# Optimization experiments

Hardware: AMD Instinct MI355X
Metric: run time of the kernel (lower is better)

## Reference

```python
import jax, jax.numpy as jnp
import numpy as np

B, N_HEADS, D_MODEL, S = 4, 16, 128, 2048
SQRT_D = np.sqrt(D_MODEL).astype(np.float32)


def setup_inputs() -> dict:
    key = jax.random.key(0)
    kx, kq, kk, kv, kw = jax.random.split(key, 5)
    N = B * N_HEADS
    return {
        "x": jax.random.normal(kx, (B, D_MODEL, S), dtype=jnp.float32),
        "Q": jax.random.normal(kq, (N, D_MODEL, S), dtype=jnp.float32),
        "K": jax.random.normal(kk, (N, D_MODEL, S), dtype=jnp.float32),
        "V": jax.random.normal(kv, (N, D_MODEL, S), dtype=jnp.float32),
        "W": jax.random.normal(kw, (N_HEADS * D_MODEL, D_MODEL), dtype=jnp.float32) * 0.02,
    }


def reference(x, Q, K, V, W):
    # x contributes only its shape (the repeated copy is overwritten in the original)
    b, d_model, s = x.shape
    # scores[n, i, j] = sum_d Q[n, d, i] * K[n, d, j] / sqrt(d_model)
    scores = jnp.einsum("ndi,ndj->nij", Q, K) / SQRT_D  # [N, S, S]
    # legacy F.softmax (no dim) on a 3D tensor -> softmax over dim=1 (query index)
    attn = jax.nn.softmax(scores, axis=1)
    # out[n, d, j] = sum_i V[n, d, i] * attn[n, i, j]
    out = jnp.einsum("ndi,nij->ndj", V, attn)  # [N, d_model, S]
    out = out.reshape(b, N_HEADS * d_model, s)  # [B, H*d_model, S]
    # final projection: W^T @ out, W: [H*d_model, d_model]
    return jnp.einsum("hd,bhs->bds", W, out)  # [B, d_model, S]
```

## Files before the change

### kernel.cpp

```cpp
#include <hip/hip_runtime.h>
#include <hip/hip_bf16.h>

typedef unsigned short u16;
typedef unsigned int   u32;
typedef short  short8v __attribute__((ext_vector_type(8)));
typedef u16    u16x8   __attribute__((ext_vector_type(8)));
typedef float  f32x16  __attribute__((ext_vector_type(16)));
typedef float  f32x4v  __attribute__((ext_vector_type(4)));
typedef u32    u32x2   __attribute__((ext_vector_type(2)));
typedef u32    u32x4   __attribute__((ext_vector_type(4)));

#define HEADS 64
#define DMODEL 128
#define SEQ 2048

#define SCQ 0.1275293f
#define PSTR 80


__device__ __forceinline__ f32x16 mfma_bf16(short8v a, short8v b, f32x16 c) {
  return __builtin_amdgcn_mfma_f32_32x32x16_bf16(a, b, c, 0, 0, 0);
}

__device__ __forceinline__ f32x16 fzero16() {
  f32x16 z;
#pragma unroll
  for (int i = 0; i < 16; ++i) z[i] = 0.f;
  return z;
}

__device__ __forceinline__ float fast_exp2(float x) {
  float r;
  asm("v_exp_f32 %0, %1" : "=v"(r) : "v"(x));
  return r;
}

__device__ __forceinline__ u32 bfround(float x) {
  u32 u = __builtin_bit_cast(u32, x);
  u += 0x7fffu + ((u >> 16) & 1u);
  return u >> 16;
}
__device__ __forceinline__ u32 bfpair(float lo, float hi) {
  u32 a = __builtin_bit_cast(u32, lo); a += 0x7fffu + ((a >> 16) & 1u);
  u32 b = __builtin_bit_cast(u32, hi); b += 0x7fffu + ((b >> 16) & 1u);
  return (a >> 16) | (b & 0xffff0000u);
}
__device__ __forceinline__ u32 packbf(float lo, float hi) {
  u32 l16 = (u32)__builtin_bit_cast(u16, __float2bfloat16(lo));
  u32 h16 = (u32)__builtin_bit_cast(u16, __float2bfloat16(hi));
  return l16 | (h16 << 16);
}

typedef const __attribute__((address_space(1))) void* gp1_t;
typedef __attribute__((address_space(3))) void* lp3_t;
__device__ __forceinline__ void gload16(const u16* g, u16* l) {
  __builtin_amdgcn_global_load_lds((gp1_t)g, (lp3_t)l, 16, 0, 0);
}

__device__ __forceinline__ void stage_T(const float* __restrict__ src, int pos0,
                                        u16* lds, int tid) {
  int ic = tid & 7;
  int d0 = (tid >> 3) * 2;
  const float* p = src + d0 * SEQ + pos0 + ic * 8;
  f32x4v xa = *reinterpret_cast<const f32x4v*>(p);
  f32x4v xb = *reinterpret_cast<const f32x4v*>(p + 4);
  f32x4v ya = *reinterpret_cast<const f32x4v*>(p + SEQ);
  f32x4v yb = *reinterpret_cast<const f32x4v*>(p + SEQ + 4);
  u32* lds32 = reinterpret_cast<u32*>(lds);
  int cc = d0 >> 3;
#pragma unroll
  for (int k = 0; k < 8; ++k) {
    int r = ic * 8 + k;
    int c2 = cc ^ (r & 15);
    float xv = (k < 4) ? xa[k & 3] : xb[k & 3];
    float yv = (k < 4) ? ya[k & 3] : yb[k & 3];
    lds32[(r * 128 + c2 * 8 + (d0 & 7)) >> 1] = bfpair(xv, yv);
  }
}

__device__ __forceinline__ short8v ld_at(const u16* lds, int row, int chunk) {
  return *reinterpret_cast<const short8v*>(lds + row * 128 + ((chunk ^ (row & 15)) * 8));
}
__device__ __forceinline__ short8v ld_vt(const u16* lds, int d, int chunk) {
  return *reinterpret_cast<const short8v*>(lds + d * 64 + ((chunk ^ (d & 7)) * 8));
}

__global__ __launch_bounds__(256) void prep_kernel(
    const float* __restrict__ Q, const float* __restrict__ V,
    const float* __restrict__ Wsrc, u16* __restrict__ Qt,
    u16* __restrict__ V16t, u16* __restrict__ Wt) {
  int blk = blockIdx.x;
  int t = threadIdx.x;
  if (blk < 2048) {
    int n = blk >> 5, pt = blk & 31;
    const float* src = Q + (size_t)n * DMODEL * SEQ;
    u16* dst = Qt + (size_t)n * SEQ * DMODEL + (size_t)pt * 64 * DMODEL;
    int pq = t & 15, dq = t >> 4;
#pragma unroll
    for (int p = 0; p < 2; ++p) {
      int d0 = (dq + 16 * p) * 4;
      const float* s0 = src + (size_t)d0 * SEQ + pt * 64 + pq * 4;
      f32x4v r0 = *reinterpret_cast<const f32x4v*>(s0);
      f32x4v r1 = *reinterpret_cast<const f32x4v*>(s0 + SEQ);
      f32x4v r2 = *reinterpret_cast<const f32x4v*>(s0 + 2 * SEQ);
      f32x4v r3 = *reinterpret_cast<const f32x4v*>(s0 + 3 * SEQ);
#pragma unroll
      for (int j = 0; j < 4; ++j) {
        u32x2 v = { bfpair(r0[j] * SCQ, r1[j] * SCQ), bfpair(r2[j] * SCQ, r3[j] * SCQ) };
        *reinterpret_cast<u32x2*>(dst + (pq * 4 + j) * DMODEL + d0) = v;
      }
    }
  } else if (blk < 4096) {
    int b2 = blk - 2048;
    int n = b2 >> 5, it = b2 & 31;
    int s8 = (t & 7) * 8;
    const float* src = V + (size_t)n * DMODEL * SEQ + it * 64 + s8;
    u16* dst = V16t + (size_t)b2 * DMODEL * 64 + s8;
#pragma unroll
    for (int rr = 0; rr < 4; ++rr) {
      int d = (t >> 3) + 32 * rr;
      const float* p = src + (size_t)d * SEQ;
      f32x4v a = *reinterpret_cast<const f32x4v*>(p);
      f32x4v b = *reinterpret_cast<const f32x4v*>(p + 4);
      u32x4 v = { bfpair(a[0], a[1]), bfpair(a[2], a[3]),
                  bfpair(b[0], b[1]), bfpair(b[2], b[3]) };
      *reinterpret_cast<u32x4*>(dst + d * 64) = v;
    }
  } else {
    int e = (blk - 4096) * 256 + t;
#pragma unroll
    for (int rr = 0; rr < 2; ++rr) {
      int o = e + rr * 131072;
      int dm = o >> 11, c = o & 2047;
      Wt[o] = (u16)bfround(Wsrc[c * 128 + dm]);
    }
  }
}

__global__ __launch_bounds__(1024, 4) void attn_kernel(
    const u16* __restrict__ Qt, const float* __restrict__ K,
    const u16* __restrict__ V16t, u16* __restrict__ Ows) {
  __shared__ __align__(16) u16 AT2[2][64 * DMODEL];
  __shared__ __align__(16) u16 VT2[2][DMODEL * 64];
  __shared__ __align__(16) u16 PB[2][256 * PSTR];
  __shared__ float AL[2][256];
  __shared__ float LL[256];
  const int tid = threadIdx.x;
  const int w = tid >> 6;
  const int lane = tid & 63;
  const int g = lane >> 5;
  const int lj = lane & 31;
  const int p_ = blockIdx.x;
  const int n = ((p_ >> 6) << 3) | (p_ & 7);
  const int j0 = ((p_ >> 3) & 7) * 256;
  const u16* Qtn = Qt + (size_t)n * SEQ * DMODEL;
  const float* Kb = K + (size_t)n * DMODEL * SEQ;
  const u16* Vtn = V16t + (size_t)n * 32 * DMODEL * 64;

  int qoff[2], voff[2];
#pragma unroll
  for (int i = 0; i < 2; ++i) {
    int idx = (w & 7) * 2 + i;
    int pos = idx * 4 + (lane >> 4);
    qoff[i] = pos * DMODEL + (((lane & 15) ^ (pos & 15)) * 8);
    int d = idx * 8 + (lane >> 3);
    voff[i] = d * 64 + (((lane & 7) ^ (d & 7)) * 8);
  }

  if (w < 8) {
    const u16* qb = Qtn;
#pragma unroll
    for (int i = 0; i < 2; ++i)
      gload16(qb + qoff[i], AT2[0] + ((w & 7) * 2 + i) * 512);
  }
  short8v bq[8];
  u16* KS = PB[0];
#pragma unroll 1
  for (int p = 0; p < 4; ++p) {
    if (tid < 512) stage_T(Kb, j0 + p * 64, KS, tid);
    __syncthreads();
    if (w < 8 && (w >> 1) == p) {
      int row = (w & 1) * 32 + lj;
#pragma unroll
      for (int c = 0; c < 8; ++c) bq[c] = ld_at(KS, row, 2 * c + g);
    }
    __syncthreads();
  }

  if (w < 8) {
    float m_run = -1e30f, l_run = 0.f;
    const int prow = w * 32 + lj;
    u16* const prowbase0 = PB[0] + prow * PSTR;
    u16* const prowbase1 = PB[1] + prow * PSTR;
    const int swz = prow & 7;

#pragma unroll 1
    for (int t = 0; t <= 32; ++t) {
      if (t < 32) {
        const u16* qb = Qtn + (size_t)((t + 1) & 31) * (64 * DMODEL);
        u16* ab = AT2[(t + 1) & 1];
#pragma unroll
        for (int i = 0; i < 2; ++i)
          gload16(qb + qoff[i], ab + ((w & 7) * 2 + i) * 512);

        const u16* curAT = AT2[t & 1];
        f32x16 c0 = fzero16(), c1 = fzero16();
        __builtin_amdgcn_s_setprio(1);
#pragma unroll
        for (int dc = 0; dc < 8; ++dc) {
          short8v a0 = ld_at(curAT, lj, 2 * dc + g);
          short8v a1 = ld_at(curAT, 32 + lj, 2 * dc + g);
          c0 = mfma_bf16(a0, bq[dc], c0);
          c1 = mfma_bf16(a1, bq[dc], c1);
        }
        __builtin_amdgcn_s_setprio(0);

        float m8[8];
#pragma unroll
        for (int r = 0; r < 8; ++r)
          m8[r] = fmaxf(fmaxf(c0[r], c0[r + 8]), fmaxf(c1[r], c1[r + 8]));
#pragma unroll
        for (int r = 0; r < 4; ++r) m8[r] = fmaxf(m8[r], m8[r + 4]);
        float mx = fmaxf(fmaxf(m8[0], m8[1]), fmaxf(m8[2], m8[3]));
        mx = fmaxf(mx, __shfl_xor(mx, 32, 64));

        float al = 1.0f;
        if (!__all(mx <= m_run + 8.f)) {
          float mn = fmaxf(m_run, mx);
          al = fast_exp2(m_run - mn);
          m_run = mn;
          l_run *= al;
        }
        if (!g) AL[t & 1][prow] = al;

#pragma unroll
        for (int r = 0; r < 16; ++r) c0[r] = fast_exp2(c0[r] - m_run);
#pragma unroll
        for (int r = 0; r < 16; ++r) c1[r] = fast_exp2(c1[r] - m_run);
        float s8[8];
#pragma unroll
        for (int r = 0; r < 8; ++r) s8[r] = (c0[r] + c0[r + 8]) + (c1[r] + c1[r + 8]);
#pragma unroll
        for (int r = 0; r < 4; ++r) s8[r] += s8[r + 4];
        float ps = (s8[0] + s8[1]) + (s8[2] + s8[3]);
        ps += __shfl_xor(ps, 32, 64);
        l_run += ps;

        u16* pdst = (t & 1) ? prowbase1 : prowbase0;
#pragma unroll
        for (int half = 0; half < 2; ++half) {
#pragma unroll
          for (int q = 0; q < 4; ++q) {
            u32x2 val;
            val.x = half ? packbf(c1[4 * q + 0], c1[4 * q + 1])
                         : packbf(c0[4 * q + 0], c0[4 * q + 1]);
            val.y = half ? packbf(c1[4 * q + 2], c1[4 * q + 3])
                         : packbf(c0[4 * q + 2], c0[4 * q + 3]);
            int G = q + 4 * half;
            *reinterpret_cast<u32x2*>(pdst + ((G ^ swz) << 3) + 4 * g) = val;
          }
        }
      }
      __syncthreads();
    }
    if (!g) LL[prow] = l_run;
    __syncthreads();
  } else {
    f32x16 o0 = fzero16(), o1 = fzero16(), o2 = fzero16(), o3 = fzero16();
    const int prow = (w - 8) * 32 + lj;
    const int swz = prow & 7;

#pragma unroll 1
    for (int t = 0; t <= 32; ++t) {
      if (t < 32) {
        const u16* vb = Vtn + (size_t)t * (DMODEL * 64);
        u16* vbuf = VT2[t & 1];
#pragma unroll
        for (int i = 0; i < 2; ++i)
          gload16(vb + voff[i], vbuf + ((w & 7) * 2 + i) * 512);
      }
      if (t >= 1) {
        const int tp = t - 1;
        const u16* curVT = VT2[tp & 1];
        const u16* prowp = PB[tp & 1] + prow * PSTR;
        float al = AL[tp & 1][prow];
        if (!__all(al == 1.0f)) {
#pragma unroll
          for (int r = 0; r < 16; ++r) { o0[r] *= al; o1[r] *= al; o2[r] *= al; o3[r] *= al; }
        }
        __builtin_amdgcn_s_setprio(1);
#pragma unroll
        for (int kc = 0; kc < 4; ++kc) {
          short8v pf = *reinterpret_cast<const short8v*>(
              prowp + (((2 * kc + g) ^ swz) << 3));
          short8v v0 = ld_vt(curVT, lj,      2 * kc + g);
          short8v v1 = ld_vt(curVT, 32 + lj, 2 * kc + g);
          short8v v2 = ld_vt(curVT, 64 + lj, 2 * kc + g);
          short8v v3 = ld_vt(curVT, 96 + lj, 2 * kc + g);
          o0 = mfma_bf16(v0, pf, o0);
          o1 = mfma_bf16(v1, pf, o1);
          o2 = mfma_bf16(v2, pf, o2);
          o3 = mfma_bf16(v3, pf, o3);
        }
        __builtin_amdgcn_s_setprio(0);
      }
      __syncthreads();
    }
    __syncthreads();
    float inv = 1.f / LL[prow];
    int jme = j0 + prow;
    u16* obase = Ows + ((size_t)n * SEQ + jme) * DMODEL;
#define STORE_OT(OV, DT)                                                  \
    {                                                                     \
      _Pragma("unroll") for (int q = 0; q < 4; ++q) {                     \
        int d0 = (DT) * 32 + 4 * g + 8 * q;                               \
        u32x2 val;                                                        \
        val.x = bfpair(OV[4 * q + 0] * inv, OV[4 * q + 1] * inv);         \
        val.y = bfpair(OV[4 * q + 2] * inv, OV[4 * q + 3] * inv);         \
        *reinterpret_cast<u32x2*>(obase + d0) = val;                      \
      }                                                                   \
    }
    STORE_OT(o0, 0) STORE_OT(o1, 1) STORE_OT(o2, 2) STORE_OT(o3, 3)
#undef STORE_OT
  }
}

__global__ __launch_bounds__(256) void proj_kernel(
    const u16* __restrict__ Ows, const u16* __restrict__ Wt, float* __restrict__ out) {
  __shared__ __align__(16) u16 BT[32 * 128];
  const int tid = threadIdx.x;
  const int w = tid >> 6, lane = tid & 63, g = lane >> 5, lj = lane & 31;
  const int b = blockIdx.x >> 6;
  const int j0 = (blockIdx.x & 63) * 32;
  f32x16 acc = fzero16();
#pragma unroll 1
  for (int h = 0; h < 16; ++h) {
    __syncthreads();
#pragma unroll
    for (int rr = 0; rr < 2; ++rr) {
      int s = tid + rr * 256;
      int r = s >> 4, cc = s & 15;
      u16x8 v = *reinterpret_cast<const u16x8*>(
          Ows + ((size_t)(b * 16 + h) * SEQ + j0 + r) * DMODEL + cc * 8);
      *reinterpret_cast<u16x8*>(BT + r * 128 + ((cc ^ (r & 7)) * 8)) = v;
    }
    __syncthreads();
#pragma unroll
    for (int kc = 0; kc < 8; ++kc) {
      short8v a = *reinterpret_cast<const short8v*>(
          Wt + (size_t)(w * 32 + lj) * SEQ + h * 128 + kc * 16 + g * 8);
      short8v bb = *reinterpret_cast<const short8v*>(
          BT + lj * 128 + (((2 * kc + g) ^ (lj & 7)) * 8));
      acc = mfma_bf16(a, bb, acc);
    }
  }
#pragma unroll
  for (int q = 0; q < 4; ++q) {
#pragma unroll
    for (int r = 0; r < 4; ++r) {
      int dm = w * 32 + 4 * g + 8 * q + r;
      out[((size_t)b * DMODEL + dm) * SEQ + j0 + lj] = acc[4 * q + r];
    }
  }
}

extern "C" void kernel_launch(void* const* d_in, const int* in_sizes, int n_in,
                              void* d_out, int out_size, void* d_ws, size_t ws_size,
                              hipStream_t stream) {
  (void)in_sizes; (void)n_in; (void)out_size; (void)ws_size;
  const float* Q = (const float*)d_in[1];
  const float* K = (const float*)d_in[2];
  const float* V = (const float*)d_in[3];
  const float* W = (const float*)d_in[4];
  const size_t NEL = (size_t)HEADS * SEQ * DMODEL;
  u16* Qt   = (u16*)d_ws;
  u16* V16t = Qt + NEL;
  u16* Ows  = V16t + NEL;
  u16* Wt   = Ows + NEL;
  float* out = (float*)d_out;

  prep_kernel<<<dim3(4608), dim3(256), 0, stream>>>(Q, V, W, Qt, V16t, Wt);
  attn_kernel<<<dim3(512), dim3(1024), 0, stream>>>(Qt, K, V16t, Ows);
  proj_kernel<<<dim3(256), dim3(256), 0, stream>>>(Ows, Wt, out);
}
```

Measured before the change: 234.7 us.

## Rebalance attention block to 4 softmax waves and 8 PV waves with 2x2 tiling

The attention block shrinks from 16 waves (8 score/softmax, 8 PV) to 12 waves: 4 producer waves each handle two 32-key column groups and process query rows in two 32-row halves, and 8 consumer waves each compute a 64x64 output tile (two key groups by two d-halves) instead of a 32x128 strip. The alpha rescale buffer gains a sub-step dimension so the consumers can apply per-half rescales. The aim is to reuse A and V fragments across two MFMAs, cut LDS reads per MFMA, and move more score work onto fewer waves with more registers each. The risk is that the 4 softmax waves become the critical path, and that occupancy drops to 3 blocks.

```diff
diff --git a/kernel.cpp b/kernel.cpp
--- a/kernel.cpp
+++ b/kernel.cpp
@@ -137,13 +137,13 @@
   }
 }
 
-__global__ __launch_bounds__(1024, 4) void attn_kernel(
+__global__ __launch_bounds__(768, 3) void attn_kernel(
     const u16* __restrict__ Qt, const float* __restrict__ K,
     const u16* __restrict__ V16t, u16* __restrict__ Ows) {
   __shared__ __align__(16) u16 AT2[2][64 * DMODEL];
   __shared__ __align__(16) u16 VT2[2][DMODEL * 64];
   __shared__ __align__(16) u16 PB[2][256 * PSTR];
-  __shared__ float AL[2][256];
+  __shared__ float AL[2][2][256];
   __shared__ float LL[256];
   const int tid = threadIdx.x;
   const int w = tid >> 6;
@@ -157,42 +157,52 @@
   const float* Kb = K + (size_t)n * DMODEL * SEQ;
   const u16* Vtn = V16t + (size_t)n * 32 * DMODEL * 64;
 
-  int qoff[2], voff[2];
-#pragma unroll
-  for (int i = 0; i < 2; ++i) {
-    int idx = (w & 7) * 2 + i;
+  int qoff[4];
+#pragma unroll
+  for (int i = 0; i < 4; ++i) {
+    int idx = (w & 3) * 4 + i;
     int pos = idx * 4 + (lane >> 4);
     qoff[i] = pos * DMODEL + (((lane & 15) ^ (pos & 15)) * 8);
+  }
+  int voff[2];
+#pragma unroll
+  for (int i = 0; i < 2; ++i) {
+    int idx = ((w - 4) & 7) * 2 + i;
     int d = idx * 8 + (lane >> 3);
     voff[i] = d * 64 + (((lane & 7) ^ (d & 7)) * 8);
   }
 
-  if (w < 8) {
-    const u16* qb = Qtn;
-#pragma unroll
-    for (int i = 0; i < 2; ++i)
-      gload16(qb + qoff[i], AT2[0] + ((w & 7) * 2 + i) * 512);
-  }
-  short8v bq[8];
+  if (w < 4) {
+#pragma unroll
+    for (int i = 0; i < 4; ++i)
+      gload16(Qtn + qoff[i], AT2[0] + ((w & 3) * 4 + i) * 512);
+  }
+
+  short8v bq0[8], bq1[8];
   u16* KS = PB[0];
 #pragma unroll 1
   for (int p = 0; p < 4; ++p) {
     if (tid < 512) stage_T(Kb, j0 + p * 64, KS, tid);
     __syncthreads();
-    if (w < 8 && (w >> 1) == p) {
+    if (w < 4) {
       int row = (w & 1) * 32 + lj;
-#pragma unroll
-      for (int c = 0; c < 8; ++c) bq[c] = ld_at(KS, row, 2 * c + g);
-    }
-    __syncthreads();
-  }
-
-  if (w < 8) {
-    float m_run = -1e30f, l_run = 0.f;
-    const int prow = w * 32 + lj;
-    u16* const prowbase0 = PB[0] + prow * PSTR;
-    u16* const prowbase1 = PB[1] + prow * PSTR;
-    const int swz = prow & 7;
+      if ((w >> 1) == p) {
+#pragma unroll
+        for (int c = 0; c < 8; ++c) bq0[c] = ld_at(KS, row, 2 * c + g);
+      }
+      if ((w >> 1) + 2 == p) {
+#pragma unroll
+        for (int c = 0; c < 8; ++c) bq1[c] = ld_at(KS, row, 2 * c + g);
+      }
+    }
+    __syncthreads();
+  }
+
+  if (w < 4) {
+    float m0 = -1e30f, l0 = 0.f, m1 = -1e30f, l1 = 0.f;
+    const int ja = w * 32 + lj;
+    const int jb = 128 + w * 32 + lj;
+    const int swza = ja & 7, swzb = jb & 7;
 
 #pragma unroll 1
     for (int t = 0; t <= 32; ++t) {
@@ -200,75 +210,74 @@
         const u16* qb = Qtn + (size_t)((t + 1) & 31) * (64 * DMODEL);
         u16* ab = AT2[(t + 1) & 1];
 #pragma unroll
-        for (int i = 0; i < 2; ++i)
-          gload16(qb + qoff[i], ab + ((w & 7) * 2 + i) * 512);
+        for (int i = 0; i < 4; ++i)
+          gload16(qb + qoff[i], ab + ((w & 3) * 4 + i) * 512);
 
         const u16* curAT = AT2[t & 1];
-        f32x16 c0 = fzero16(), c1 = fzero16();
-        __builtin_amdgcn_s_setprio(1);
-#pragma unroll
-        for (int dc = 0; dc < 8; ++dc) {
-          short8v a0 = ld_at(curAT, lj, 2 * dc + g);
-          short8v a1 = ld_at(curAT, 32 + lj, 2 * dc + g);
-          c0 = mfma_bf16(a0, bq[dc], c0);
-          c1 = mfma_bf16(a1, bq[dc], c1);
+        u16* pda = PB[t & 1] + ja * PSTR;
+        u16* pdb = PB[t & 1] + jb * PSTR;
+
+#pragma unroll
+        for (int s = 0; s < 2; ++s) {
+          f32x16 c0 = fzero16(), c1 = fzero16();
+          __builtin_amdgcn_s_setprio(1);
+#pragma unroll
+          for (int dc = 0; dc < 8; ++dc) {
+            short8v a = ld_at(curAT, s * 32 + lj, 2 * dc + g);
+            c0 = mfma_bf16(a, bq0[dc], c0);
+            c1 = mfma_bf16(a, bq1[dc], c1);
+          }
+          __builtin_amdgcn_s_setprio(0);
+
+#define SOFTPACK(C, M, L, JROW, SWZ, PD)                                     \
+          {                                                                  \
+            float t8[8];                                                     \
+            _Pragma("unroll") for (int r = 0; r < 8; ++r)                    \
+                t8[r] = fmaxf(C[r], C[r + 8]);                               \
+            _Pragma("unroll") for (int r = 0; r < 4; ++r)                    \
+                t8[r] = fmaxf(t8[r], t8[r + 4]);                             \
+            float mx = fmaxf(fmaxf(t8[0], t8[1]), fmaxf(t8[2], t8[3]));      \
+            mx = fmaxf(mx, __shfl_xor(mx, 32, 64));                          \
+            float al = 1.0f;                                                 \
+            if (!__all(mx <= (M) + 8.f)) {                                   \
+              float mn = fmaxf((M), mx);                                     \
+              al = fast_exp2((M)-mn);                                        \
+              (M) = mn; (L) *= al;                                           \
+            }                                                                \
+            if (!g) AL[t & 1][s][JROW] = al;                                 \
+            _Pragma("unroll") for (int r = 0; r < 16; ++r)                   \
+                C[r] = fast_exp2(C[r] - (M));                                \
+            _Pragma("unroll") for (int r = 0; r < 8; ++r)                    \
+                t8[r] = C[r] + C[r + 8];                                     \
+            _Pragma("unroll") for (int r = 0; r < 4; ++r)                    \
+                t8[r] += t8[r + 4];                                          \
+            float ps = (t8[0] + t8[1]) + (t8[2] + t8[3]);                    \
+            ps += __shfl_xor(ps, 32, 64);                                    \
+            (L) += ps;                                                       \
+            _Pragma("unroll") for (int q = 0; q < 4; ++q) {                  \
+              u32x2 val = { packbf(C[4 * q + 0], C[4 * q + 1]),              \
+                            packbf(C[4 * q + 2], C[4 * q + 3]) };            \
+              *reinterpret_cast<u32x2*>(                                     \
+                  (PD) + (((4 * s + q) ^ (SWZ)) << 3) + 4 * g) = val;        \
+            }                                                                \
+          }
+          SOFTPACK(c0, m0, l0, ja, swza, pda)
+          SOFTPACK(c1, m1, l1, jb, swzb, pdb)
+#undef SOFTPACK
         }
-        __builtin_amdgcn_s_setprio(0);
-
-        float m8[8];
-#pragma unroll
-        for (int r = 0; r < 8; ++r)
-          m8[r] = fmaxf(fmaxf(c0[r], c0[r + 8]), fmaxf(c1[r], c1[r + 8]));
-#pragma unroll
-        for (int r = 0; r < 4; ++r) m8[r] = fmaxf(m8[r], m8[r + 4]);
-        float mx = fmaxf(fmaxf(m8[0], m8[1]), fmaxf(m8[2], m8[3]));
-        mx = fmaxf(mx, __shfl_xor(mx, 32, 64));
-
-        float al = 1.0f;
-        if (!__all(mx <= m_run + 8.f)) {
-          float mn = fmaxf(m_run, mx);
-          al = fast_exp2(m_run - mn);
-          m_run = mn;
-          l_run *= al;
-        }
-        if (!g) AL[t & 1][prow] = al;
-
-#pragma unroll
-        for (int r = 0; r < 16; ++r) c0[r] = fast_exp2(c0[r] - m_run);
-#pragma unroll
-        for (int r = 0; r < 16; ++r) c1[r] = fast_exp2(c1[r] - m_run);
-        float s8[8];
-#pragma unroll
-        for (int r = 0; r < 8; ++r) s8[r] = (c0[r] + c0[r + 8]) + (c1[r] + c1[r + 8]);
-#pragma unroll
-        for (int r = 0; r < 4; ++r) s8[r] += s8[r + 4];
-        float ps = (s8[0] + s8[1]) + (s8[2] + s8[3]);
-        ps += __shfl_xor(ps, 32, 64);
-        l_run += ps;
-
-        u16* pdst = (t & 1) ? prowbase1 : prowbase0;
-#pragma unroll
-        for (int half = 0; half < 2; ++half) {
-#pragma unroll
-          for (int q = 0; q < 4; ++q) {
-            u32x2 val;
-            val.x = half ? packbf(c1[4 * q + 0], c1[4 * q + 1])
-                         : packbf(c0[4 * q + 0], c0[4 * q + 1]);
-            val.y = half ? packbf(c1[4 * q + 2], c1[4 * q + 3])
-                         : packbf(c0[4 * q + 2], c0[4 * q + 3]);
-            int G = q + 4 * half;
-            *reinterpret_cast<u32x2*>(pdst + ((G ^ swz) << 3) + 4 * g) = val;
-          }
-        }
       }
       __syncthreads();
     }
-    if (!g) LL[prow] = l_run;
+    if (!g) { LL[ja] = l0; LL[jb] = l1; }
     __syncthreads();
   } else {
-    f32x16 o0 = fzero16(), o1 = fzero16(), o2 = fzero16(), o3 = fzero16();
-    const int prow = (w - 8) * 32 + lj;
-    const int swz = prow & 7;
+    f32x16 oa0 = fzero16(), oa1 = fzero16(), ob0 = fzero16(), ob1 = fzero16();
+    const int cw = w - 4;
+    const int u = cw & 3, dh = cw >> 2;
+    const int ja = 64 * u + lj;
+    const int jb = ja + 32;
+    const int swza = ja & 7, swzb = jb & 7;
+    const int dbase = dh * 64;
 
 #pragma unroll 1
     for (int t = 0; t <= 32; ++t) {
@@ -277,50 +286,58 @@
         u16* vbuf = VT2[t & 1];
 #pragma unroll
         for (int i = 0; i < 2; ++i)
-          gload16(vb + voff[i], vbuf + ((w & 7) * 2 + i) * 512);
+          gload16(vb + voff[i], vbuf + (cw * 2 + i) * 512);
       }
       if (t >= 1) {
         const int tp = t - 1;
         const u16* curVT = VT2[tp & 1];
-        const u16* prowp = PB[tp & 1] + prow * PSTR;
-        float al = AL[tp & 1][prow];
-        if (!__all(al == 1.0f)) {
-#pragma unroll
-          for (int r = 0; r < 16; ++r) { o0[r] *= al; o1[r] *= al; o2[r] *= al; o3[r] *= al; }
+        const u16* pa = PB[tp & 1] + ja * PSTR;
+        const u16* pb = PB[tp & 1] + jb * PSTR;
+#pragma unroll
+        for (int s = 0; s < 2; ++s) {
+          float ala = AL[tp & 1][s][ja];
+          float alb = AL[tp & 1][s][jb];
+          if (!__all((ala == 1.0f) && (alb == 1.0f))) {
+#pragma unroll
+            for (int r = 0; r < 16; ++r) {
+              oa0[r] *= ala; oa1[r] *= ala; ob0[r] *= alb; ob1[r] *= alb;
+            }
+          }
+          __builtin_amdgcn_s_setprio(1);
+#pragma unroll
+          for (int kl = 0; kl < 2; ++kl) {
+            int G = 4 * s + 2 * kl + g;
+            short8v pfa = *reinterpret_cast<const short8v*>(pa + ((G ^ swza) << 3));
+            short8v pfb = *reinterpret_cast<const short8v*>(pb + ((G ^ swzb) << 3));
+            short8v v0 = ld_vt(curVT, dbase + lj, G);
+            short8v v1 = ld_vt(curVT, dbase + 32 + lj, G);
+            oa0 = mfma_bf16(v0, pfa, oa0);
+            oa1 = mfma_bf16(v1, pfa, oa1);
+            ob0 = mfma_bf16(v0, pfb, ob0);
+            ob1 = mfma_bf16(v1, pfb, ob1);
+          }
+          __builtin_amdgcn_s_setprio(0);
         }
-        __builtin_amdgcn_s_setprio(1);
-#pragma unroll
-        for (int kc = 0; kc < 4; ++kc) {
-          short8v pf = *reinterpret_cast<const short8v*>(
-              prowp + (((2 * kc + g) ^ swz) << 3));
-          short8v v0 = ld_vt(curVT, lj,      2 * kc + g);
-          short8v v1 = ld_vt(curVT, 32 + lj, 2 * kc + g);
-          short8v v2 = ld_vt(curVT, 64 + lj, 2 * kc + g);
-          short8v v3 = ld_vt(curVT, 96 + lj, 2 * kc + g);
-          o0 = mfma_bf16(v0, pf, o0);
-          o1 = mfma_bf16(v1, pf, o1);
-          o2 = mfma_bf16(v2, pf, o2);
-          o3 = mfma_bf16(v3, pf, o3);
-        }
-        __builtin_amdgcn_s_setprio(0);
       }
       __syncthreads();
     }
     __syncthreads();
-    float inv = 1.f / LL[prow];
-    int jme = j0 + prow;
-    u16* obase = Ows + ((size_t)n * SEQ + jme) * DMODEL;
-#define STORE_OT(OV, DT)                                                  \
+    float inva = 1.f / LL[ja];
+    float invb = 1.f / LL[jb];
+    u16* obase_a = Ows + ((size_t)n * SEQ + j0 + ja) * DMODEL;
+    u16* obase_b = Ows + ((size_t)n * SEQ + j0 + jb) * DMODEL;
+#define STORE_OT(OV, OB, DB, INV)                                         \
     {                                                                     \
       _Pragma("unroll") for (int q = 0; q < 4; ++q) {                     \
-        int d0 = (DT) * 32 + 4 * g + 8 * q;                               \
+        int d0 = dbase + (DB) * 32 + 4 * g + 8 * q;                       \
         u32x2 val;                                                        \
-        val.x = bfpair(OV[4 * q + 0] * inv, OV[4 * q + 1] * inv);         \
-        val.y = bfpair(OV[4 * q + 2] * inv, OV[4 * q + 3] * inv);         \
-        *reinterpret_cast<u32x2*>(obase + d0) = val;                      \
+        val.x = bfpair(OV[4 * q + 0] * (INV), OV[4 * q + 1] * (INV));     \
+        val.y = bfpair(OV[4 * q + 2] * (INV), OV[4 * q + 3] * (INV));     \
+        *reinterpret_cast<u32x2*>((OB) + d0) = val;                       \
       }                                                                   \
     }
-    STORE_OT(o0, 0) STORE_OT(o1, 1) STORE_OT(o2, 2) STORE_OT(o3, 3)
+    STORE_OT(oa0, obase_a, 0, inva) STORE_OT(oa1, obase_a, 1, inva)
+    STORE_OT(ob0, obase_b, 0, invb) STORE_OT(ob1, obase_b, 1, invb)
 #undef STORE_OT
   }
 }
@@ -380,6 +397,6 @@
   float* out = (float*)d_out;
 
   prep_kernel<<<dim3(4608), dim3(256), 0, stream>>>(Q, V, W, Qt, V16t, Wt);
-  attn_kernel<<<dim3(512), dim3(1024), 0, stream>>>(Qt, K, V16t, Ows);
+  attn_kernel<<<dim3(512), dim3(768), 0, stream>>>(Qt, K, V16t, Ows);
   proj_kernel<<<dim3(256), dim3(256), 0, stream>>>(Ows, Wt, out);
 }
```

Result: slower. 266.4 us (+13.5%).

## Halve attention block tiles to 512 threads with 32-row Q and V steps

Applied to the files above, without the earlier changes.

Each attention block now handles 128 key columns instead of 256, runs 512 threads (4 softmax waves, 4 PV waves), and steps through the query dimension in 32-row tiles over 64 iterations. The V prep layout becomes 32-wide tiles with a new swizzle, and the PV waves each cover two column groups and half of d_model so V fragments are reused. The grid doubles to 1024 blocks to improve occupancy and load balance and to shrink LDS per block, at the cost of twice as many loop iterations and barriers per block.

```diff
diff --git a/kernel.cpp b/kernel.cpp
--- a/kernel.cpp
+++ b/kernel.cpp
@@ -15,7 +15,7 @@
 #define SEQ 2048
 
 #define SCQ 0.1275293f
-#define PSTR 80
+#define PSTR 40
 
 
 __device__ __forceinline__ f32x16 mfma_bf16(short8v a, short8v b, f32x16 c) {
@@ -81,8 +81,9 @@
 __device__ __forceinline__ short8v ld_at(const u16* lds, int row, int chunk) {
   return *reinterpret_cast<const short8v*>(lds + row * 128 + ((chunk ^ (row & 15)) * 8));
 }
-__device__ __forceinline__ short8v ld_vt(const u16* lds, int d, int chunk) {
-  return *reinterpret_cast<const short8v*>(lds + d * 64 + ((chunk ^ (d & 7)) * 8));
+__device__ __forceinline__ short8v ld_vt32(const u16* lds, int d, int G) {
+  return *reinterpret_cast<const short8v*>(
+      lds + d * 32 + ((G ^ ((d ^ (d >> 2)) & 3)) * 8));
 }
 
 __global__ __launch_bounds__(256) void prep_kernel(
@@ -112,19 +113,19 @@
     }
   } else if (blk < 4096) {
     int b2 = blk - 2048;
-    int n = b2 >> 5, it = b2 & 31;
-    int s8 = (t & 7) * 8;
-    const float* src = V + (size_t)n * DMODEL * SEQ + it * 64 + s8;
-    u16* dst = V16t + (size_t)b2 * DMODEL * 64 + s8;
-#pragma unroll
-    for (int rr = 0; rr < 4; ++rr) {
-      int d = (t >> 3) + 32 * rr;
-      const float* p = src + (size_t)d * SEQ;
-      f32x4v a = *reinterpret_cast<const f32x4v*>(p);
-      f32x4v b = *reinterpret_cast<const f32x4v*>(p + 4);
+    int n = b2 >> 5, tp = b2 & 31;
+    int tile = tp * 2 + (t >> 7);
+    int d = t & 127;
+    const float* src = V + ((size_t)n * DMODEL + d) * SEQ + tile * 32;
+    u16* dst = V16t + (((size_t)n * 64 + tile) * DMODEL + d) * 32;
+    u32x4* dst16 = reinterpret_cast<u32x4*>(dst);
+#pragma unroll
+    for (int c = 0; c < 4; ++c) {
+      f32x4v a = *reinterpret_cast<const f32x4v*>(src + c * 8);
+      f32x4v b = *reinterpret_cast<const f32x4v*>(src + c * 8 + 4);
       u32x4 v = { bfpair(a[0], a[1]), bfpair(a[2], a[3]),
                   bfpair(b[0], b[1]), bfpair(b[2], b[3]) };
-      *reinterpret_cast<u32x4*>(dst + d * 64) = v;
+      dst16[c] = v;
     }
   } else {
     int e = (blk - 4096) * 256 + t;
@@ -137,49 +138,49 @@
   }
 }
 
-__global__ __launch_bounds__(1024, 4) void attn_kernel(
+__global__ __launch_bounds__(512, 4) void attn_kernel(
     const u16* __restrict__ Qt, const float* __restrict__ K,
     const u16* __restrict__ V16t, u16* __restrict__ Ows) {
-  __shared__ __align__(16) u16 AT2[2][64 * DMODEL];
-  __shared__ __align__(16) u16 VT2[2][DMODEL * 64];
-  __shared__ __align__(16) u16 PB[2][256 * PSTR];
-  __shared__ float AL[2][256];
-  __shared__ float LL[256];
+  __shared__ __align__(16) u16 AT2[2][32 * DMODEL];
+  __shared__ __align__(16) u16 VT2[2][DMODEL * 32];
+  __shared__ __align__(16) u16 PB[2][128 * PSTR];
+  __shared__ float AL[2][128];
+  __shared__ float LL[128];
   const int tid = threadIdx.x;
   const int w = tid >> 6;
   const int lane = tid & 63;
   const int g = lane >> 5;
   const int lj = lane & 31;
   const int p_ = blockIdx.x;
-  const int n = ((p_ >> 6) << 3) | (p_ & 7);
-  const int j0 = ((p_ >> 3) & 7) * 256;
+  const int n = ((p_ >> 7) << 3) | (p_ & 7);
+  const int j0 = ((p_ >> 3) & 15) * 128;
   const u16* Qtn = Qt + (size_t)n * SEQ * DMODEL;
   const float* Kb = K + (size_t)n * DMODEL * SEQ;
-  const u16* Vtn = V16t + (size_t)n * 32 * DMODEL * 64;
+  const u16* Vtn = V16t + (size_t)n * 64 * DMODEL * 32;
 
   int qoff[2], voff[2];
 #pragma unroll
   for (int i = 0; i < 2; ++i) {
-    int idx = (w & 7) * 2 + i;
+    int idx = (w & 3) * 2 + i;
     int pos = idx * 4 + (lane >> 4);
     qoff[i] = pos * DMODEL + (((lane & 15) ^ (pos & 15)) * 8);
-    int d = idx * 8 + (lane >> 3);
-    voff[i] = d * 64 + (((lane & 7) ^ (d & 7)) * 8);
-  }
-
-  if (w < 8) {
-    const u16* qb = Qtn;
+    int d = idx * 16 + (lane >> 2);
+    voff[i] = d * 32 + (((lane & 3) ^ ((d ^ (d >> 2)) & 3)) * 8);
+  }
+
+  if (w < 4) {
 #pragma unroll
     for (int i = 0; i < 2; ++i)
-      gload16(qb + qoff[i], AT2[0] + ((w & 7) * 2 + i) * 512);
-  }
+      gload16(Qtn + qoff[i], AT2[0] + ((w & 3) * 2 + i) * 512);
+  }
+
   short8v bq[8];
   u16* KS = PB[0];
 #pragma unroll 1
-  for (int p = 0; p < 4; ++p) {
-    if (tid < 512) stage_T(Kb, j0 + p * 64, KS, tid);
-    __syncthreads();
-    if (w < 8 && (w >> 1) == p) {
+  for (int p = 0; p < 2; ++p) {
+    stage_T(Kb, j0 + p * 64, KS, tid);
+    __syncthreads();
+    if (w < 4 && (w >> 1) == p) {
       int row = (w & 1) * 32 + lj;
 #pragma unroll
       for (int c = 0; c < 8; ++c) bq[c] = ld_at(KS, row, 2 * c + g);
@@ -187,41 +188,36 @@
     __syncthreads();
   }
 
-  if (w < 8) {
+  if (w < 4) {
     float m_run = -1e30f, l_run = 0.f;
-    const int prow = w * 32 + lj;
-    u16* const prowbase0 = PB[0] + prow * PSTR;
-    u16* const prowbase1 = PB[1] + prow * PSTR;
-    const int swz = prow & 7;
+    const int jrow = w * 32 + lj;
+    const int rotj = (jrow ^ (jrow >> 2)) & 3;
 
 #pragma unroll 1
-    for (int t = 0; t <= 32; ++t) {
-      if (t < 32) {
-        const u16* qb = Qtn + (size_t)((t + 1) & 31) * (64 * DMODEL);
+    for (int t = 0; t <= 64; ++t) {
+      if (t < 64) {
+        const u16* qb = Qtn + (size_t)((t + 1) & 63) * (32 * DMODEL);
         u16* ab = AT2[(t + 1) & 1];
 #pragma unroll
         for (int i = 0; i < 2; ++i)
-          gload16(qb + qoff[i], ab + ((w & 7) * 2 + i) * 512);
+          gload16(qb + qoff[i], ab + ((w & 3) * 2 + i) * 512);
 
         const u16* curAT = AT2[t & 1];
-        f32x16 c0 = fzero16(), c1 = fzero16();
+        f32x16 c0 = fzero16();
         __builtin_amdgcn_s_setprio(1);
 #pragma unroll
         for (int dc = 0; dc < 8; ++dc) {
-          short8v a0 = ld_at(curAT, lj, 2 * dc + g);
-          short8v a1 = ld_at(curAT, 32 + lj, 2 * dc + g);
-          c0 = mfma_bf16(a0, bq[dc], c0);
-          c1 = mfma_bf16(a1, bq[dc], c1);
+          short8v a = ld_at(curAT, lj, 2 * dc + g);
+          c0 = mfma_bf16(a, bq[dc], c0);
         }
         __builtin_amdgcn_s_setprio(0);
 
-        float m8[8];
-#pragma unroll
-        for (int r = 0; r < 8; ++r)
-          m8[r] = fmaxf(fmaxf(c0[r], c0[r + 8]), fmaxf(c1[r], c1[r + 8]));
-#pragma unroll
-        for (int r = 0; r < 4; ++r) m8[r] = fmaxf(m8[r], m8[r + 4]);
-        float mx = fmaxf(fmaxf(m8[0], m8[1]), fmaxf(m8[2], m8[3]));
+        float t8[8];
+#pragma unroll
+        for (int r = 0; r < 8; ++r) t8[r] = fmaxf(c0[r], c0[r + 8]);
+#pragma unroll
+        for (int r = 0; r < 4; ++r) t8[r] = fmaxf(t8[r], t8[r + 4]);
+        float mx = fmaxf(fmaxf(t8[0], t8[1]), fmaxf(t8[2], t8[3]));
         mx = fmaxf(mx, __shfl_xor(mx, 32, 64));
 
         float al = 1.0f;
@@ -231,96 +227,96 @@
           m_run = mn;
           l_run *= al;
         }
-        if (!g) AL[t & 1][prow] = al;
+        if (!g) AL[t & 1][jrow] = al;
 
 #pragma unroll
         for (int r = 0; r < 16; ++r) c0[r] = fast_exp2(c0[r] - m_run);
 #pragma unroll
-        for (int r = 0; r < 16; ++r) c1[r] = fast_exp2(c1[r] - m_run);
-        float s8[8];
-#pragma unroll
-        for (int r = 0; r < 8; ++r) s8[r] = (c0[r] + c0[r + 8]) + (c1[r] + c1[r + 8]);
-#pragma unroll
-        for (int r = 0; r < 4; ++r) s8[r] += s8[r + 4];
-        float ps = (s8[0] + s8[1]) + (s8[2] + s8[3]);
+        for (int r = 0; r < 8; ++r) t8[r] = c0[r] + c0[r + 8];
+#pragma unroll
+        for (int r = 0; r < 4; ++r) t8[r] += t8[r + 4];
+        float ps = (t8[0] + t8[1]) + (t8[2] + t8[3]);
         ps += __shfl_xor(ps, 32, 64);
         l_run += ps;
 
-        u16* pdst = (t & 1) ? prowbase1 : prowbase0;
-#pragma unroll
-        for (int half = 0; half < 2; ++half) {
-#pragma unroll
-          for (int q = 0; q < 4; ++q) {
-            u32x2 val;
-            val.x = half ? packbf(c1[4 * q + 0], c1[4 * q + 1])
-                         : packbf(c0[4 * q + 0], c0[4 * q + 1]);
-            val.y = half ? packbf(c1[4 * q + 2], c1[4 * q + 3])
-                         : packbf(c0[4 * q + 2], c0[4 * q + 3]);
-            int G = q + 4 * half;
-            *reinterpret_cast<u32x2*>(pdst + ((G ^ swz) << 3) + 4 * g) = val;
-          }
+        u16* pdst = PB[t & 1] + jrow * PSTR;
+#pragma unroll
+        for (int q = 0; q < 4; ++q) {
+          u32x2 val = { packbf(c0[4 * q + 0], c0[4 * q + 1]),
+                        packbf(c0[4 * q + 2], c0[4 * q + 3]) };
+          *reinterpret_cast<u32x2*>(pdst + ((q ^ rotj) << 3) + 4 * g) = val;
         }
       }
       __syncthreads();
     }
-    if (!g) LL[prow] = l_run;
+    if (!g) LL[jrow] = l_run;
     __syncthreads();
   } else {
-    f32x16 o0 = fzero16(), o1 = fzero16(), o2 = fzero16(), o3 = fzero16();
-    const int prow = (w - 8) * 32 + lj;
-    const int swz = prow & 7;
+    f32x16 oa0 = fzero16(), oa1 = fzero16(), ob0 = fzero16(), ob1 = fzero16();
+    const int cw = w - 4;
+    const int u = cw & 1, dh = cw >> 1;
+    const int ja = 64 * u + lj;
+    const int jb = ja + 32;
+    const int rota = (ja ^ (ja >> 2)) & 3;
+    const int rotb = (jb ^ (jb >> 2)) & 3;
+    const int dbase = dh * 64;
 
 #pragma unroll 1
-    for (int t = 0; t <= 32; ++t) {
-      if (t < 32) {
-        const u16* vb = Vtn + (size_t)t * (DMODEL * 64);
+    for (int t = 0; t <= 64; ++t) {
+      if (t < 64) {
+        const u16* vb = Vtn + (size_t)t * (DMODEL * 32);
         u16* vbuf = VT2[t & 1];
 #pragma unroll
         for (int i = 0; i < 2; ++i)
-          gload16(vb + voff[i], vbuf + ((w & 7) * 2 + i) * 512);
+          gload16(vb + voff[i], vbuf + (cw * 2 + i) * 512);
       }
       if (t >= 1) {
         const int tp = t - 1;
         const u16* curVT = VT2[tp & 1];
-        const u16* prowp = PB[tp & 1] + prow * PSTR;
-        float al = AL[tp & 1][prow];
-        if (!__all(al == 1.0f)) {
-#pragma unroll
-          for (int r = 0; r < 16; ++r) { o0[r] *= al; o1[r] *= al; o2[r] *= al; o3[r] *= al; }
+        const u16* pa = PB[tp & 1] + ja * PSTR;
+        const u16* pb = PB[tp & 1] + jb * PSTR;
+        float ala = AL[tp & 1][ja];
+        float alb = AL[tp & 1][jb];
+        if (!__all((ala == 1.0f) && (alb == 1.0f))) {
+#pragma unroll
+          for (int r = 0; r < 16; ++r) {
+            oa0[r] *= ala; oa1[r] *= ala; ob0[r] *= alb; ob1[r] *= alb;
+          }
         }
         __builtin_amdgcn_s_setprio(1);
 #pragma unroll
-        for (int kc = 0; kc < 4; ++kc) {
-          short8v pf = *reinterpret_cast<const short8v*>(
-              prowp + (((2 * kc + g) ^ swz) << 3));
-          short8v v0 = ld_vt(curVT, lj,      2 * kc + g);
-          short8v v1 = ld_vt(curVT, 32 + lj, 2 * kc + g);
-          short8v v2 = ld_vt(curVT, 64 + lj, 2 * kc + g);
-          short8v v3 = ld_vt(curVT, 96 + lj, 2 * kc + g);
-          o0 = mfma_bf16(v0, pf, o0);
-          o1 = mfma_bf16(v1, pf, o1);
-          o2 = mfma_bf16(v2, pf, o2);
-          o3 = mfma_bf16(v3, pf, o3);
+        for (int kc = 0; kc < 2; ++kc) {
+          int G = 2 * kc + g;
+          short8v pfa = *reinterpret_cast<const short8v*>(pa + ((G ^ rota) << 3));
+          short8v pfb = *reinterpret_cast<const short8v*>(pb + ((G ^ rotb) << 3));
+          short8v v0 = ld_vt32(curVT, dbase + lj, G);
+          short8v v1 = ld_vt32(curVT, dbase + 32 + lj, G);
+          oa0 = mfma_bf16(v0, pfa, oa0);
+          oa1 = mfma_bf16(v1, pfa, oa1);
+          ob0 = mfma_bf16(v0, pfb, ob0);
+          ob1 = mfma_bf16(v1, pfb, ob1);
         }
         __builtin_amdgcn_s_setprio(0);
       }
       __syncthreads();
     }
     __syncthreads();
-    float inv = 1.f / LL[prow];
-    int jme = j0 + prow;
-    u16* obase = Ows + ((size_t)n * SEQ + jme) * DMODEL;
-#define STORE_OT(OV, DT)                                                  \
+    float inva = 1.f / LL[ja];
+    float invb = 1.f / LL[jb];
+    u16* obase_a = Ows + ((size_t)n * SEQ + j0 + ja) * DMODEL;
+    u16* obase_b = Ows + ((size_t)n * SEQ + j0 + jb) * DMODEL;
+#define STORE_OT(OV, OB, DT, INV)                                         \
     {                                                                     \
       _Pragma("unroll") for (int q = 0; q < 4; ++q) {                     \
-        int d0 = (DT) * 32 + 4 * g + 8 * q;                               \
+        int d0 = dbase + (DT) * 32 + 4 * g + 8 * q;                       \
         u32x2 val;                                                        \
-        val.x = bfpair(OV[4 * q + 0] * inv, OV[4 * q + 1] * inv);         \
-        val.y = bfpair(OV[4 * q + 2] * inv, OV[4 * q + 3] * inv);         \
-        *reinterpret_cast<u32x2*>(obase + d0) = val;                      \
+        val.x = bfpair(OV[4 * q + 0] * (INV), OV[4 * q + 1] * (INV));     \
+        val.y = bfpair(OV[4 * q + 2] * (INV), OV[4 * q + 3] * (INV));     \
+        *reinterpret_cast<u32x2*>((OB) + d0) = val;                       \
       }                                                                   \
     }
-    STORE_OT(o0, 0) STORE_OT(o1, 1) STORE_OT(o2, 2) STORE_OT(o3, 3)
+    STORE_OT(oa0, obase_a, 0, inva) STORE_OT(oa1, obase_a, 1, inva)
+    STORE_OT(ob0, obase_b, 0, invb) STORE_OT(ob1, obase_b, 1, invb)
 #undef STORE_OT
   }
 }
@@ -380,6 +376,6 @@
   float* out = (float*)d_out;
 
   prep_kernel<<<dim3(4608), dim3(256), 0, stream>>>(Q, V, W, Qt, V16t, Wt);
-  attn_kernel<<<dim3(512), dim3(1024), 0, stream>>>(Qt, K, V16t, Ows);
+  attn_kernel<<<dim3(1024), dim3(512), 0, stream>>>(Qt, K, V16t, Ows);
   proj_kernel<<<dim3(256), dim3(256), 0, stream>>>(Ows, Wt, out);
 }
```

After: 251.8 us. 1.07x slower.
